# Kernel optimization log

Hardware: AMD Instinct MI355X
Metric: run time of the kernel (lower is better)

## Reference

```python
import jax, jax.numpy as jnp
import numpy as np

HEADS = 8
DIM_HEAD = 32
DIM = 256
HIDDEN = HEADS * DIM_HEAD  # 256


def setup_inputs() -> dict:
    key = jax.random.key(0)
    ks = jax.random.split(key, 6)
    B, T, C, H, W = 4, 16, DIM, 32, 32
    x = jax.random.normal(ks[0], (B, T, C, H, W), dtype=jnp.float32)
    rel_pos = jax.random.normal(ks[1], (HEADS, T, T), dtype=jnp.float32)
    # 1x1 conv weights == channel-mixing matrices
    w_qkv = jax.random.normal(ks[2], (3 * HIDDEN, C), dtype=jnp.float32) * (C ** -0.5)
    b_qkv = jnp.zeros((3 * HIDDEN,), dtype=jnp.float32)
    w_out = jax.random.normal(ks[3], (C, HIDDEN), dtype=jnp.float32) * (HIDDEN ** -0.5)
    b_out = jnp.zeros((C,), dtype=jnp.float32)
    return {"x": x, "rel_pos": rel_pos, "w_qkv": w_qkv, "b_qkv": b_qkv,
            "w_out": w_out, "b_out": b_out}


def reference(x, rel_pos, w_qkv, b_qkv, w_out, b_out):
    B, T, C, H, W = x.shape
    scale = DIM_HEAD ** -0.5
    # 1x1 conv QKV projection: (B,T,C,H,W) x (3*hidden, C) -> (B,T,H,W,3*hidden)
    qkv = jnp.einsum('btchw,oc->bthwo', x, w_qkv) + b_qkv
    q, k, v = jnp.split(qkv, 3, axis=-1)
    # split heads: (B,T,H,W,heads,dim_head); attention over T per (b,h,w,head)
    q = q.reshape(B, T, H, W, HEADS, DIM_HEAD) * scale
    k = k.reshape(B, T, H, W, HEADS, DIM_HEAD)
    v = v.reshape(B, T, H, W, HEADS, DIM_HEAD)
    # sim: (B,H,W,heads,T,T)
    sim = jnp.einsum('bihwnd,bjhwnd->bhwnij', q, k)
    sim = sim + rel_pos  # (heads,T,T) broadcasts over (B,H,W)
    attn = jax.nn.softmax(sim, axis=-1)
    out = jnp.einsum('bhwnij,bjhwnd->bihwnd', attn, v)  # (B,T,H,W,heads,dh)
    out = out.reshape(B, T, H, W, HIDDEN)
    # 1x1 conv output projection back to C channels
    y = jnp.einsum('bthwe,ce->bthwc', out, w_out) + b_out
    return jnp.transpose(y, (0, 1, 4, 2, 3))  # (B,T,C,H,W)
```

## Files before the change

kernel.cpp:

```cpp
#include <hip/hip_runtime.h>
#include <hip/hip_bf16.h>

typedef __attribute__((ext_vector_type(8))) short bf16x8;
typedef __attribute__((ext_vector_type(4))) float f32x4;
typedef __attribute__((ext_vector_type(16))) float f32x16;

namespace {

__device__ __forceinline__ unsigned short f2bf(float f) {
  unsigned int x;
  __builtin_memcpy(&x, &f, 4);
  x += 0x7fff + ((x >> 16) & 1);
  return (unsigned short)(x >> 16);
}
__device__ __forceinline__ unsigned int pack2(float a, float b) {
  return (unsigned int)f2bf(a) | ((unsigned int)f2bf(b) << 16);
}

constexpr int kWBStride = 264;
constexpr int kWBTile = 32 * kWBStride;
constexpr int kWB = 2 * kWBTile;
constexpr int kSite = 1920;
constexpr int kSmem = kWB + 8 * kSite;
constexpr int kPanelStride = 72;
constexpr int kWTileOff = 17408;
static_assert(kSmem * 2 <= 65536, "LDS budget");
static_assert(16 * 16 * kPanelStride <= kSmem, "x panel fits");
static_assert(512 * 17 * 4 <= kSmem * 2, "fbuf fits");
static_assert(kWTileOff + kWBTile <= kSmem, "wout tile fits after fbuf");

__global__ __launch_bounds__(512, 1) void attn_fused(
    const float* __restrict__ x,
    const float* __restrict__ rel,
    const float* __restrict__ wqkv,
    const float* __restrict__ bqkv,
    const float* __restrict__ wout,
    const float* __restrict__ bout,
    float* __restrict__ out) {
  __shared__ __align__(16) unsigned short smem[kSmem];
  const int tid = threadIdx.x;
  const int lane = tid & 63;
  const int wave = tid >> 6;
  const int quad = lane >> 4;
  const int lrow = lane & 15;
  const int half = lane >> 5;
  const int n32 = lane & 31;
  const int b = blockIdx.x >> 6;
  const int hw0 = (blockIdx.x & 63) * 16;

  const int wrow = tid >> 4;
  const int wcol = (tid & 15) * 16;
  float4 pw[4];
  {
    const float* sp = wqkv + (size_t)wrow * 256 + wcol;
#pragma unroll
    for (int u = 0; u < 4; ++u) pw[u] = *(const float4*)(sp + u * 4);
  }

  bf16x8 ax[16];
  {
    unsigned short* panel = smem;
    const int sloc = wave * 2 + (n32 >> 4);
#pragma unroll
    for (int cc4 = 0; cc4 < 4; ++cc4) {
      const int c0 = cc4 * 64;
      __syncthreads();
#pragma unroll
      for (int u = 0; u < 8; ++u) {
        const int idx = u * 512 + tid;
        const int row = idx >> 2;
        const int q = idx & 3;
        const int t = row >> 6;
        const int cl = row & 63;
        const float4 v = *(const float4*)(
            x + (((size_t)(b * 16 + t) * 256 + c0 + cl) << 10) + hw0 + q * 4);
        unsigned short* pr = panel + (t * 16 + q * 4) * kPanelStride + cl;
        pr[0] = f2bf(v.x);
        pr[kPanelStride] = f2bf(v.y);
        pr[2 * kPanelStride] = f2bf(v.z);
        pr[3 * kPanelStride] = f2bf(v.w);
      }
      __syncthreads();
#pragma unroll
      for (int kk = 0; kk < 4; ++kk)
        ax[cc4 * 4 + kk] = *(const bf16x8*)(
            panel + (lrow * 16 + sloc) * kPanelStride + kk * 16 + half * 8);
    }
  }

  unsigned short* qb = smem + kWB + wave * kSite;
  unsigned short* kb = qb + 640;
  unsigned short* vt = qb + 1280;

  const f32x4 zero4 = {0.f, 0.f, 0.f, 0.f};
  const float scale = 0.17677669529663687f;
  bf16x8 ao[2][8];

  auto qkv_tile = [&](int g, float bias) -> f32x16 {
    __syncthreads();
    unsigned short* WBc = smem + (g & 1) * kWBTile;
    {
      unsigned short* dst = WBc + wrow * kWBStride + wcol;
      uint4 a, bq;
      a.x = pack2(pw[0].x, pw[0].y);
      a.y = pack2(pw[0].z, pw[0].w);
      a.z = pack2(pw[1].x, pw[1].y);
      a.w = pack2(pw[1].z, pw[1].w);
      bq.x = pack2(pw[2].x, pw[2].y);
      bq.y = pack2(pw[2].z, pw[2].w);
      bq.z = pack2(pw[3].x, pw[3].y);
      bq.w = pack2(pw[3].z, pw[3].w);
      *(uint4*)dst = a;
      *(uint4*)(dst + 8) = bq;
    }
    {
      const int gn = g + 1;
      const int rowbase = (gn % 3) * 256 + (gn / 3) * 32;
      const float* sp = wqkv + (size_t)(rowbase + wrow) * 256 + wcol;
#pragma unroll
      for (int u = 0; u < 4; ++u) pw[u] = *(const float4*)(sp + u * 4);
    }
    __syncthreads();
    f32x16 accA, accB;
#pragma unroll
    for (int i = 0; i < 16; ++i) { accA[i] = bias; accB[i] = 0.f; }
    const unsigned short* br = WBc + n32 * kWBStride + half * 8;
#pragma unroll
    for (int kp = 0; kp < 8; ++kp) {
      const bf16x8 bfa = *(const bf16x8*)(br + (2 * kp) * 16);
      const bf16x8 bfb = *(const bf16x8*)(br + (2 * kp + 1) * 16);
      accA = __builtin_amdgcn_mfma_f32_32x32x16_bf16(ax[2 * kp], bfa, accA, 0, 0, 0);
      accB = __builtin_amdgcn_mfma_f32_32x32x16_bf16(ax[2 * kp + 1], bfb, accB, 0, 0, 0);
    }
#pragma unroll
    for (int i = 0; i < 16; ++i) accA[i] += accB[i];
    return accA;
  };

  auto head_body = [&](int h) {
    const f32x16 qacc = qkv_tile(h * 3 + 0, bqkv[h * 32 + n32]);
    const f32x16 kacc = qkv_tile(h * 3 + 1, bqkv[256 + h * 32 + n32]);
    const f32x16 vacc = qkv_tile(h * 3 + 2, bqkv[512 + h * 32 + n32]);
    float rl[4];
#pragma unroll
    for (int r = 0; r < 4; ++r) rl[r] = rel[h * 256 + (quad * 4 + r) * 16 + lrow];

#pragma unroll
    for (int s = 0; s < 2; ++s) {
#pragma unroll
      for (int rr = 0; rr < 8; ++rr) {
        const int t = (rr & 3) + 8 * (rr >> 2) + 4 * half;
        qb[t * 40 + n32] = f2bf(qacc[8 * s + rr]);
        kb[t * 40 + n32] = f2bf(kacc[8 * s + rr]);
      }
#pragma unroll
      for (int rp = 0; rp < 4; ++rp) {
        const int rr = rp * 2;
        const int t = (rr & 3) + 8 * (rr >> 2) + 4 * half;
        *(unsigned int*)&vt[n32 * 20 + t] =
            pack2(vacc[8 * s + rr], vacc[8 * s + rr + 1]);
      }
      const bf16x8 qf = *(const bf16x8*)(qb + lrow * 40 + quad * 8);
      const bf16x8 kf = *(const bf16x8*)(kb + lrow * 40 + quad * 8);
      const f32x4 sim = __builtin_amdgcn_mfma_f32_16x16x32_bf16(qf, kf, zero4, 0, 0, 0);
      float p[4], inv[4];
#pragma unroll
      for (int r = 0; r < 4; ++r) {
        const float v = sim[r] * scale + rl[r];
        float m = v;
        for (int off = 8; off; off >>= 1) m = fmaxf(m, __shfl_xor(m, off));
        const float e = __expf(v - m);
        float sum = e;
        for (int off = 8; off; off >>= 1) sum += __shfl_xor(sum, off);
        p[r] = e;
        inv[r] = 1.0f / sum;
      }
      unsigned short* pb = kb;
#pragma unroll
      for (int r = 0; r < 4; ++r) pb[(quad * 4 + r) * 24 + lrow] = f2bf(p[r]);
      bf16x8 pf, vf0, vf1;
      if (quad < 2) {
        pf = *(const bf16x8*)(pb + lrow * 24 + quad * 8);
        vf0 = *(const bf16x8*)(vt + lrow * 20 + quad * 8);
        vf1 = *(const bf16x8*)(vt + (16 + lrow) * 20 + quad * 8);
      } else {
#pragma unroll
        for (int j = 0; j < 8; ++j) { pf[j] = 0; vf0[j] = 0; vf1[j] = 0; }
      }
      const f32x4 o0 = __builtin_amdgcn_mfma_f32_16x16x32_bf16(pf, vf0, zero4, 0, 0, 0);
      const f32x4 o1 = __builtin_amdgcn_mfma_f32_16x16x32_bf16(pf, vf1, zero4, 0, 0, 0);
#pragma unroll
      for (int r = 0; r < 4; ++r) {
        const int t = quad * 4 + r;
        qb[t * 40 + lrow] = f2bf(o0[r] * inv[r]);
        qb[t * 40 + 16 + lrow] = f2bf(o1[r] * inv[r]);
      }
      ao[s][h] = *(const bf16x8*)(qb + lrow * 40 + quad * 8);
    }
  };

  head_body(0);
  head_body(1);
  head_body(2);
  head_body(3);
  head_body(4);
  head_body(5);
  head_body(6);
  head_body(7);

  __syncthreads();
  float* fbuf = (float*)smem;
  unsigned short* wtile = smem + kWTileOff;
  float* ob = out + ((size_t)b << 22);
#pragma unroll 1
  for (int cc = 0; cc < 8; ++cc) {
    {
      const float* sp = wout + (size_t)(cc * 32 + wrow) * 256 + wcol;
      const float4 v0 = ((const float4*)sp)[0];
      const float4 v1 = ((const float4*)sp)[1];
      const float4 v2 = ((const float4*)sp)[2];
      const float4 v3 = ((const float4*)sp)[3];
      uint4 a, bq;
      a.x = pack2(v0.x, v0.y);
      a.y = pack2(v0.z, v0.w);
      a.z = pack2(v1.x, v1.y);
      a.w = pack2(v1.z, v1.w);
      bq.x = pack2(v2.x, v2.y);
      bq.y = pack2(v2.z, v2.w);
      bq.z = pack2(v3.x, v3.y);
      bq.w = pack2(v3.z, v3.w);
      unsigned short* d = wtile + wrow * kWBStride + wcol;
      *(uint4*)d = a;
      *(uint4*)(d + 8) = bq;
    }
    __syncthreads();
#pragma unroll
    for (int sub = 0; sub < 2; ++sub) {
      const int c = cc * 32 + sub * 16 + lrow;
      const float bias = bout[c];
      f32x4 y0 = {bias, bias, bias, bias};
      f32x4 y1 = {bias, bias, bias, bias};
      const unsigned short* wrow_p = wtile + (sub * 16 + lrow) * kWBStride;
#pragma unroll
      for (int ks = 0; ks < 8; ++ks) {
        const bf16x8 wf = *(const bf16x8*)(wrow_p + ks * 32 + quad * 8);
        y0 = __builtin_amdgcn_mfma_f32_16x16x32_bf16(ao[0][ks], wf, y0, 0, 0, 0);
        y1 = __builtin_amdgcn_mfma_f32_16x16x32_bf16(ao[1][ks], wf, y1, 0, 0, 0);
      }
#pragma unroll
      for (int r = 0; r < 4; ++r) {
        const int t = quad * 4 + r;
        const int L = (t * 32 + sub * 16 + lrow) * 17 + wave * 2;
        fbuf[L] = y0[r];
        fbuf[L + 1] = y1[r];
      }
    }
    __syncthreads();
    {
      const int t = tid >> 5, cl = tid & 31;
      float v[16];
#pragma unroll
      for (int i = 0; i < 16; ++i) v[i] = fbuf[tid * 17 + i];
      float* dst = ob + ((size_t)(t * 256 + cc * 32 + cl)) * 1024 + hw0;
#pragma unroll
      for (int u = 0; u < 4; ++u) {
        float4 q;
        q.x = v[u * 4]; q.y = v[u * 4 + 1]; q.z = v[u * 4 + 2]; q.w = v[u * 4 + 3];
        *(float4*)(dst + u * 4) = q;
      }
    }
    __syncthreads();
  }
}

}

extern "C" void kernel_launch(void* const* d_in, const int* in_sizes, int n_in,
                              void* d_out, int out_size, void* d_ws, size_t ws_size,
                              hipStream_t stream) {
  const float* x = (const float*)d_in[0];
  const float* rel = (const float*)d_in[1];
  const float* wqkv = (const float*)d_in[2];
  const float* bqkv = (const float*)d_in[3];
  const float* wout = (const float*)d_in[4];
  const float* bout = (const float*)d_in[5];
  float* out = (float*)d_out;
  (void)in_sizes; (void)n_in; (void)out_size; (void)d_ws; (void)ws_size;

  attn_fused<<<256, 512, 0, stream>>>(x, rel, wqkv, bqkv, wout, bout, out);
}
```

Measured before the change: 202.5 us.

## Pre-convert weights to bf16 workspace and read MFMA operands directly from L2

After: 261.2 us. 29.0% more time.

```diff
diff --git a/kernel.cpp b/kernel.cpp
--- a/kernel.cpp
+++ b/kernel.cpp
@@ -17,25 +17,236 @@
   return (unsigned int)f2bf(a) | ((unsigned int)f2bf(b) << 16);
 }
 
+__global__ __launch_bounds__(256) void wprep(const float* __restrict__ wqkv,
+                                             const float* __restrict__ wout,
+                                             unsigned short* __restrict__ wAll) {
+  const int g = blockIdx.x;
+  const int tid = threadIdx.x;
+  const int row_l = tid >> 3;
+  const int seg = tid & 7;
+  const float* src;
+  int srow;
+  if (g < 24) { src = wqkv; srow = (g % 3) * 256 + (g / 3) * 32 + row_l; }
+  else        { src = wout; srow = (g - 24) * 32 + row_l; }
+  const float* s = src + (size_t)srow * 256 + seg * 32;
+  unsigned short* d = wAll + ((size_t)(g * 32 + row_l)) * 256 + seg * 32;
+#pragma unroll
+  for (int u = 0; u < 8; ++u) {
+    const float4 v = *(const float4*)(s + u * 4);
+    uint2 p;
+    p.x = pack2(v.x, v.y);
+    p.y = pack2(v.z, v.w);
+    *(uint2*)(d + u * 4) = p;
+  }
+}
+
+constexpr int kPanelStride = 72;
+constexpr int kPanel = 16 * 16 * kPanelStride;
+constexpr int kSiteL = 1920;
+constexpr int kSmemL = kPanel + 8 * kSiteL;
+static_assert(512 * 17 * 4 <= kPanel * 2, "fbuf fits in panel region");
+
+__global__ __launch_bounds__(512, 1) void attn_l2w(
+    const float* __restrict__ x,
+    const float* __restrict__ rel,
+    const unsigned short* __restrict__ wAll,
+    const float* __restrict__ bqkv,
+    const float* __restrict__ bout,
+    float* __restrict__ out) {
+  __shared__ __align__(16) unsigned short smem[kSmemL];
+  const int tid = threadIdx.x;
+  const int lane = tid & 63;
+  const int wave = tid >> 6;
+  const int quad = lane >> 4;
+  const int lrow = lane & 15;
+  const int half = lane >> 5;
+  const int n32 = lane & 31;
+  const int b = blockIdx.x >> 6;
+  const int hw0 = (blockIdx.x & 63) * 16;
+
+  bf16x8 ax[16];
+  {
+    unsigned short* panel = smem;
+    const int sloc = wave * 2 + (n32 >> 4);
+#pragma unroll
+    for (int cc4 = 0; cc4 < 4; ++cc4) {
+      const int c0 = cc4 * 64;
+      __syncthreads();
+#pragma unroll
+      for (int u = 0; u < 8; ++u) {
+        const int idx = u * 512 + tid;
+        const int row = idx >> 2;
+        const int q = idx & 3;
+        const int t = row >> 6;
+        const int cl = row & 63;
+        const float4 v = *(const float4*)(
+            x + (((size_t)(b * 16 + t) * 256 + c0 + cl) << 10) + hw0 + q * 4);
+        unsigned short* pr = panel + (t * 16 + q * 4) * kPanelStride + cl;
+        pr[0] = f2bf(v.x);
+        pr[kPanelStride] = f2bf(v.y);
+        pr[2 * kPanelStride] = f2bf(v.z);
+        pr[3 * kPanelStride] = f2bf(v.w);
+      }
+      __syncthreads();
+#pragma unroll
+      for (int kk = 0; kk < 4; ++kk)
+        ax[cc4 * 4 + kk] = *(const bf16x8*)(
+            panel + (lrow * 16 + sloc) * kPanelStride + kk * 16 + half * 8);
+    }
+  }
+
+  unsigned short* qb = smem + kPanel + wave * kSiteL;
+  unsigned short* kb = qb + 640;
+  unsigned short* vt = qb + 1280;
+
+  const f32x4 zero4 = {0.f, 0.f, 0.f, 0.f};
+  const float scale = 0.17677669529663687f;
+  bf16x8 ao[2][8];
+
+  auto qkv_tile = [&](int g, float bias) -> f32x16 {
+    f32x16 accA, accB;
+#pragma unroll
+    for (int i = 0; i < 16; ++i) { accA[i] = bias; accB[i] = 0.f; }
+    const unsigned short* br = wAll + (((size_t)(g * 32 + n32)) << 8) + half * 8;
+#pragma unroll
+    for (int kp = 0; kp < 8; ++kp) {
+      const bf16x8 bfa = *(const bf16x8*)(br + (2 * kp) * 16);
+      const bf16x8 bfb = *(const bf16x8*)(br + (2 * kp + 1) * 16);
+      accA = __builtin_amdgcn_mfma_f32_32x32x16_bf16(ax[2 * kp], bfa, accA, 0, 0, 0);
+      accB = __builtin_amdgcn_mfma_f32_32x32x16_bf16(ax[2 * kp + 1], bfb, accB, 0, 0, 0);
+    }
+#pragma unroll
+    for (int i = 0; i < 16; ++i) accA[i] += accB[i];
+    return accA;
+  };
+
+  auto head_body = [&](int h) {
+    const f32x16 qacc = qkv_tile(h * 3 + 0, bqkv[h * 32 + n32]);
+    const f32x16 kacc = qkv_tile(h * 3 + 1, bqkv[256 + h * 32 + n32]);
+    const f32x16 vacc = qkv_tile(h * 3 + 2, bqkv[512 + h * 32 + n32]);
+    float rl[4];
+#pragma unroll
+    for (int r = 0; r < 4; ++r) rl[r] = rel[h * 256 + (quad * 4 + r) * 16 + lrow];
+
+#pragma unroll
+    for (int s = 0; s < 2; ++s) {
+#pragma unroll
+      for (int rr = 0; rr < 8; ++rr) {
+        const int t = (rr & 3) + 8 * (rr >> 2) + 4 * half;
+        qb[t * 40 + n32] = f2bf(qacc[8 * s + rr]);
+        kb[t * 40 + n32] = f2bf(kacc[8 * s + rr]);
+      }
+#pragma unroll
+      for (int rp = 0; rp < 4; ++rp) {
+        const int rr = rp * 2;
+        const int t = (rr & 3) + 8 * (rr >> 2) + 4 * half;
+        *(unsigned int*)&vt[n32 * 20 + t] =
+            pack2(vacc[8 * s + rr], vacc[8 * s + rr + 1]);
+      }
+      const bf16x8 qf = *(const bf16x8*)(qb + lrow * 40 + quad * 8);
+      const bf16x8 kf = *(const bf16x8*)(kb + lrow * 40 + quad * 8);
+      const f32x4 sim = __builtin_amdgcn_mfma_f32_16x16x32_bf16(qf, kf, zero4, 0, 0, 0);
+      float p[4], inv[4];
+#pragma unroll
+      for (int r = 0; r < 4; ++r) {
+        const float v = sim[r] * scale + rl[r];
+        float m = v;
+        for (int off = 8; off; off >>= 1) m = fmaxf(m, __shfl_xor(m, off));
+        const float e = __expf(v - m);
+        float sum = e;
+        for (int off = 8; off; off >>= 1) sum += __shfl_xor(sum, off);
+        p[r] = e;
+        inv[r] = 1.0f / sum;
+      }
+      unsigned short* pb = kb;
+#pragma unroll
+      for (int r = 0; r < 4; ++r) pb[(quad * 4 + r) * 24 + lrow] = f2bf(p[r]);
+      bf16x8 pf, vf0, vf1;
+      if (quad < 2) {
+        pf = *(const bf16x8*)(pb + lrow * 24 + quad * 8);
+        vf0 = *(const bf16x8*)(vt + lrow * 20 + quad * 8);
+        vf1 = *(const bf16x8*)(vt + (16 + lrow) * 20 + quad * 8);
+      } else {
+#pragma unroll
+        for (int j = 0; j < 8; ++j) { pf[j] = 0; vf0[j] = 0; vf1[j] = 0; }
+      }
+      const f32x4 o0 = __builtin_amdgcn_mfma_f32_16x16x32_bf16(pf, vf0, zero4, 0, 0, 0);
+      const f32x4 o1 = __builtin_amdgcn_mfma_f32_16x16x32_bf16(pf, vf1, zero4, 0, 0, 0);
+#pragma unroll
+      for (int r = 0; r < 4; ++r) {
+        const int t = quad * 4 + r;
+        qb[t * 40 + lrow] = f2bf(o0[r] * inv[r]);
+        qb[t * 40 + 16 + lrow] = f2bf(o1[r] * inv[r]);
+      }
+      ao[s][h] = *(const bf16x8*)(qb + lrow * 40 + quad * 8);
+    }
+  };
+
+  head_body(0);
+  head_body(1);
+  head_body(2);
+  head_body(3);
+  head_body(4);
+  head_body(5);
+  head_body(6);
+  head_body(7);
+
+  __syncthreads();
+  float* fbuf = (float*)smem;
+  float* ob = out + ((size_t)b << 22);
+#pragma unroll 1
+  for (int cc = 0; cc < 8; ++cc) {
+#pragma unroll
+    for (int sub = 0; sub < 2; ++sub) {
+      const int c = cc * 32 + sub * 16 + lrow;
+      const float bias = bout[c];
+      f32x4 y0 = {bias, bias, bias, bias};
+      f32x4 y1 = {bias, bias, bias, bias};
+#pragma unroll
+      for (int ks = 0; ks < 8; ++ks) {
+        const bf16x8 wf =
+            *(const bf16x8*)(wAll + (size_t)(768 + c) * 256 + ks * 32 + quad * 8);
+        y0 = __builtin_amdgcn_mfma_f32_16x16x32_bf16(ao[0][ks], wf, y0, 0, 0, 0);
+        y1 = __builtin_amdgcn_mfma_f32_16x16x32_bf16(ao[1][ks], wf, y1, 0, 0, 0);
+      }
+#pragma unroll
+      for (int r = 0; r < 4; ++r) {
+        const int t = quad * 4 + r;
+        const int L = (t * 32 + sub * 16 + lrow) * 17 + wave * 2;
+        fbuf[L] = y0[r];
+        fbuf[L + 1] = y1[r];
+      }
+    }
+    __syncthreads();
+    {
+      const int t = tid >> 5, cl = tid & 31;
+      float v[16];
+#pragma unroll
+      for (int i = 0; i < 16; ++i) v[i] = fbuf[tid * 17 + i];
+      float* dst = ob + ((size_t)(t * 256 + cc * 32 + cl)) * 1024 + hw0;
+#pragma unroll
+      for (int u = 0; u < 4; ++u) {
+        float4 q;
+        q.x = v[u * 4]; q.y = v[u * 4 + 1]; q.z = v[u * 4 + 2]; q.w = v[u * 4 + 3];
+        *(float4*)(dst + u * 4) = q;
+      }
+    }
+    __syncthreads();
+  }
+}
+
 constexpr int kWBStride = 264;
 constexpr int kWBTile = 32 * kWBStride;
 constexpr int kWB = 2 * kWBTile;
 constexpr int kSite = 1920;
 constexpr int kSmem = kWB + 8 * kSite;
-constexpr int kPanelStride = 72;
 constexpr int kWTileOff = 17408;
-static_assert(kSmem * 2 <= 65536, "LDS budget");
-static_assert(16 * 16 * kPanelStride <= kSmem, "x panel fits");
-static_assert(512 * 17 * 4 <= kSmem * 2, "fbuf fits");
-static_assert(kWTileOff + kWBTile <= kSmem, "wout tile fits after fbuf");
+static_assert(kSmem * 2 <= 160 * 1024, "LDS budget");
 
 __global__ __launch_bounds__(512, 1) void attn_fused(
-    const float* __restrict__ x,
-    const float* __restrict__ rel,
-    const float* __restrict__ wqkv,
-    const float* __restrict__ bqkv,
-    const float* __restrict__ wout,
-    const float* __restrict__ bout,
+    const float* __restrict__ x, const float* __restrict__ rel,
+    const float* __restrict__ wqkv, const float* __restrict__ bqkv,
+    const float* __restrict__ wout, const float* __restrict__ bout,
     float* __restrict__ out) {
   __shared__ __align__(16) unsigned short smem[kSmem];
   const int tid = threadIdx.x;
@@ -285,7 +496,14 @@
   const float* wout = (const float*)d_in[4];
   const float* bout = (const float*)d_in[5];
   float* out = (float*)d_out;
-  (void)in_sizes; (void)n_in; (void)out_size; (void)d_ws; (void)ws_size;
-
-  attn_fused<<<256, 512, 0, stream>>>(x, rel, wqkv, bqkv, wout, bout, out);
-}
+  (void)in_sizes; (void)n_in; (void)out_size;
+
+  constexpr size_t kWAllBytes = (size_t)1024 * 256 * sizeof(unsigned short);
+  if (ws_size >= kWAllBytes) {
+    unsigned short* wAll = (unsigned short*)d_ws;
+    wprep<<<32, 256, 0, stream>>>(wqkv, wout, wAll);
+    attn_l2w<<<256, 512, 0, stream>>>(x, rel, wAll, bqkv, bout, out);
+  } else {
+    attn_fused<<<256, 512, 0, stream>>>(x, rel, wqkv, bqkv, wout, bout, out);
+  }
+}
```

## Use 1024-thread blocks with one spatial site per wave and 16x16 MFMAs

Applied to the files above, without the earlier changes.

Result: no change. 203.3 us (+0.4%).

```diff
diff --git a/kernel.cpp b/kernel.cpp
--- a/kernel.cpp
+++ b/kernel.cpp
@@ -3,7 +3,6 @@
 
 typedef __attribute__((ext_vector_type(8))) short bf16x8;
 typedef __attribute__((ext_vector_type(4))) float f32x4;
-typedef __attribute__((ext_vector_type(16))) float f32x16;
 
 namespace {
 
@@ -20,16 +19,16 @@
 constexpr int kWBStride = 264;
 constexpr int kWBTile = 32 * kWBStride;
 constexpr int kWB = 2 * kWBTile;
-constexpr int kSite = 1920;
-constexpr int kSmem = kWB + 8 * kSite;
+constexpr int kSite = 1792;
+constexpr int kSmem = kWB + 16 * kSite;
 constexpr int kPanelStride = 72;
-constexpr int kWTileOff = 17408;
-static_assert(kSmem * 2 <= 65536, "LDS budget");
+constexpr int kWTileOff = 34816;
+static_assert(kSmem * 2 <= 160 * 1024, "LDS budget");
 static_assert(16 * 16 * kPanelStride <= kSmem, "x panel fits");
 static_assert(512 * 17 * 4 <= kSmem * 2, "fbuf fits");
 static_assert(kWTileOff + kWBTile <= kSmem, "wout tile fits after fbuf");
 
-__global__ __launch_bounds__(512, 1) void attn_fused(
+__global__ __launch_bounds__(1024, 4) void attn_fused(
     const float* __restrict__ x,
     const float* __restrict__ rel,
     const float* __restrict__ wqkv,
@@ -43,31 +42,28 @@
   const int wave = tid >> 6;
   const int quad = lane >> 4;
   const int lrow = lane & 15;
-  const int half = lane >> 5;
-  const int n32 = lane & 31;
   const int b = blockIdx.x >> 6;
   const int hw0 = (blockIdx.x & 63) * 16;
 
-  const int wrow = tid >> 4;
-  const int wcol = (tid & 15) * 16;
-  float4 pw[4];
+  const int wrow = tid >> 5;
+  const int wcol = (tid & 31) * 8;
+  float4 pw[2];
   {
     const float* sp = wqkv + (size_t)wrow * 256 + wcol;
-#pragma unroll
-    for (int u = 0; u < 4; ++u) pw[u] = *(const float4*)(sp + u * 4);
+    pw[0] = ((const float4*)sp)[0];
+    pw[1] = ((const float4*)sp)[1];
   }
 
-  bf16x8 ax[16];
+  bf16x8 ax[8];
   {
     unsigned short* panel = smem;
-    const int sloc = wave * 2 + (n32 >> 4);
 #pragma unroll
     for (int cc4 = 0; cc4 < 4; ++cc4) {
       const int c0 = cc4 * 64;
       __syncthreads();
 #pragma unroll
-      for (int u = 0; u < 8; ++u) {
-        const int idx = u * 512 + tid;
+      for (int u = 0; u < 4; ++u) {
+        const int idx = u * 1024 + tid;
         const int row = idx >> 2;
         const int q = idx & 3;
         const int t = row >> 6;
@@ -82,121 +78,112 @@
       }
       __syncthreads();
 #pragma unroll
-      for (int kk = 0; kk < 4; ++kk)
-        ax[cc4 * 4 + kk] = *(const bf16x8*)(
-            panel + (lrow * 16 + sloc) * kPanelStride + kk * 16 + half * 8);
+      for (int kk = 0; kk < 2; ++kk)
+        ax[cc4 * 2 + kk] = *(const bf16x8*)(
+            panel + (lrow * 16 + wave) * kPanelStride + kk * 32 + quad * 8);
     }
   }
 
   unsigned short* qb = smem + kWB + wave * kSite;
-  unsigned short* kb = qb + 640;
-  unsigned short* vt = qb + 1280;
+  unsigned short* kbuf = qb + 512;
+  unsigned short* vtb = qb + 1024;
+  unsigned short* pb = qb + 1536;
 
   const f32x4 zero4 = {0.f, 0.f, 0.f, 0.f};
   const float scale = 0.17677669529663687f;
-  bf16x8 ao[2][8];
-
-  auto qkv_tile = [&](int g, float bias) -> f32x16 {
+  bf16x8 ao[8];
+
+  auto qkv_tile = [&](int g, int h, int sel) {
     __syncthreads();
     unsigned short* WBc = smem + (g & 1) * kWBTile;
     {
-      unsigned short* dst = WBc + wrow * kWBStride + wcol;
-      uint4 a, bq;
+      uint4 a;
       a.x = pack2(pw[0].x, pw[0].y);
       a.y = pack2(pw[0].z, pw[0].w);
       a.z = pack2(pw[1].x, pw[1].y);
       a.w = pack2(pw[1].z, pw[1].w);
-      bq.x = pack2(pw[2].x, pw[2].y);
-      bq.y = pack2(pw[2].z, pw[2].w);
-      bq.z = pack2(pw[3].x, pw[3].y);
-      bq.w = pack2(pw[3].z, pw[3].w);
-      *(uint4*)dst = a;
-      *(uint4*)(dst + 8) = bq;
+      *(uint4*)(WBc + wrow * kWBStride + wcol) = a;
     }
     {
       const int gn = g + 1;
       const int rowbase = (gn % 3) * 256 + (gn / 3) * 32;
       const float* sp = wqkv + (size_t)(rowbase + wrow) * 256 + wcol;
-#pragma unroll
-      for (int u = 0; u < 4; ++u) pw[u] = *(const float4*)(sp + u * 4);
-    }
-    __syncthreads();
-    f32x16 accA, accB;
-#pragma unroll
-    for (int i = 0; i < 16; ++i) { accA[i] = bias; accB[i] = 0.f; }
-    const unsigned short* br = WBc + n32 * kWBStride + half * 8;
-#pragma unroll
-    for (int kp = 0; kp < 8; ++kp) {
-      const bf16x8 bfa = *(const bf16x8*)(br + (2 * kp) * 16);
-      const bf16x8 bfb = *(const bf16x8*)(br + (2 * kp + 1) * 16);
-      accA = __builtin_amdgcn_mfma_f32_32x32x16_bf16(ax[2 * kp], bfa, accA, 0, 0, 0);
-      accB = __builtin_amdgcn_mfma_f32_32x32x16_bf16(ax[2 * kp + 1], bfb, accB, 0, 0, 0);
-    }
-#pragma unroll
-    for (int i = 0; i < 16; ++i) accA[i] += accB[i];
-    return accA;
+      pw[0] = ((const float4*)sp)[0];
+      pw[1] = ((const float4*)sp)[1];
+    }
+    __syncthreads();
+    const float bias0 = bqkv[sel * 256 + h * 32 + lrow];
+    const float bias1 = bqkv[sel * 256 + h * 32 + 16 + lrow];
+    f32x4 acc0 = {bias0, bias0, bias0, bias0};
+    f32x4 acc1 = {bias1, bias1, bias1, bias1};
+#pragma unroll
+    for (int ks = 0; ks < 8; ++ks) {
+      const bf16x8 b0 =
+          *(const bf16x8*)(WBc + lrow * kWBStride + ks * 32 + quad * 8);
+      const bf16x8 b1 =
+          *(const bf16x8*)(WBc + (16 + lrow) * kWBStride + ks * 32 + quad * 8);
+      acc0 = __builtin_amdgcn_mfma_f32_16x16x32_bf16(ax[ks], b0, acc0, 0, 0, 0);
+      acc1 = __builtin_amdgcn_mfma_f32_16x16x32_bf16(ax[ks], b1, acc1, 0, 0, 0);
+    }
+    if (sel < 2) {
+      unsigned short* dst = sel ? kbuf : qb;
+#pragma unroll
+      for (int r = 0; r < 4; ++r) {
+        const int row = quad * 4 + r;
+        dst[row * 32 + lrow] = f2bf(acc0[r]);
+        dst[row * 32 + 16 + lrow] = f2bf(acc1[r]);
+      }
+    } else {
+#pragma unroll
+      for (int r = 0; r < 4; ++r) {
+        const int row = quad * 4 + r;
+        vtb[lrow * 16 + row] = f2bf(acc0[r]);
+        vtb[(16 + lrow) * 16 + row] = f2bf(acc1[r]);
+      }
+    }
   };
 
   auto head_body = [&](int h) {
-    const f32x16 qacc = qkv_tile(h * 3 + 0, bqkv[h * 32 + n32]);
-    const f32x16 kacc = qkv_tile(h * 3 + 1, bqkv[256 + h * 32 + n32]);
-    const f32x16 vacc = qkv_tile(h * 3 + 2, bqkv[512 + h * 32 + n32]);
-    float rl[4];
-#pragma unroll
-    for (int r = 0; r < 4; ++r) rl[r] = rel[h * 256 + (quad * 4 + r) * 16 + lrow];
-
-#pragma unroll
-    for (int s = 0; s < 2; ++s) {
-#pragma unroll
-      for (int rr = 0; rr < 8; ++rr) {
-        const int t = (rr & 3) + 8 * (rr >> 2) + 4 * half;
-        qb[t * 40 + n32] = f2bf(qacc[8 * s + rr]);
-        kb[t * 40 + n32] = f2bf(kacc[8 * s + rr]);
-      }
-#pragma unroll
-      for (int rp = 0; rp < 4; ++rp) {
-        const int rr = rp * 2;
-        const int t = (rr & 3) + 8 * (rr >> 2) + 4 * half;
-        *(unsigned int*)&vt[n32 * 20 + t] =
-            pack2(vacc[8 * s + rr], vacc[8 * s + rr + 1]);
-      }
-      const bf16x8 qf = *(const bf16x8*)(qb + lrow * 40 + quad * 8);
-      const bf16x8 kf = *(const bf16x8*)(kb + lrow * 40 + quad * 8);
-      const f32x4 sim = __builtin_amdgcn_mfma_f32_16x16x32_bf16(qf, kf, zero4, 0, 0, 0);
-      float p[4], inv[4];
-#pragma unroll
-      for (int r = 0; r < 4; ++r) {
-        const float v = sim[r] * scale + rl[r];
-        float m = v;
-        for (int off = 8; off; off >>= 1) m = fmaxf(m, __shfl_xor(m, off));
-        const float e = __expf(v - m);
-        float sum = e;
-        for (int off = 8; off; off >>= 1) sum += __shfl_xor(sum, off);
-        p[r] = e;
-        inv[r] = 1.0f / sum;
-      }
-      unsigned short* pb = kb;
-#pragma unroll
-      for (int r = 0; r < 4; ++r) pb[(quad * 4 + r) * 24 + lrow] = f2bf(p[r]);
-      bf16x8 pf, vf0, vf1;
-      if (quad < 2) {
-        pf = *(const bf16x8*)(pb + lrow * 24 + quad * 8);
-        vf0 = *(const bf16x8*)(vt + lrow * 20 + quad * 8);
-        vf1 = *(const bf16x8*)(vt + (16 + lrow) * 20 + quad * 8);
-      } else {
-#pragma unroll
-        for (int j = 0; j < 8; ++j) { pf[j] = 0; vf0[j] = 0; vf1[j] = 0; }
-      }
-      const f32x4 o0 = __builtin_amdgcn_mfma_f32_16x16x32_bf16(pf, vf0, zero4, 0, 0, 0);
-      const f32x4 o1 = __builtin_amdgcn_mfma_f32_16x16x32_bf16(pf, vf1, zero4, 0, 0, 0);
-#pragma unroll
-      for (int r = 0; r < 4; ++r) {
-        const int t = quad * 4 + r;
-        qb[t * 40 + lrow] = f2bf(o0[r] * inv[r]);
-        qb[t * 40 + 16 + lrow] = f2bf(o1[r] * inv[r]);
-      }
-      ao[s][h] = *(const bf16x8*)(qb + lrow * 40 + quad * 8);
-    }
+    qkv_tile(h * 3 + 0, h, 0);
+    qkv_tile(h * 3 + 1, h, 1);
+    qkv_tile(h * 3 + 2, h, 2);
+
+    const bf16x8 qf = *(const bf16x8*)&qb[lrow * 32 + quad * 8];
+    const bf16x8 kf = *(const bf16x8*)&kbuf[lrow * 32 + quad * 8];
+    const f32x4 sim = __builtin_amdgcn_mfma_f32_16x16x32_bf16(qf, kf, zero4, 0, 0, 0);
+    float p[4], inv[4];
+#pragma unroll
+    for (int r = 0; r < 4; ++r) {
+      const int i = quad * 4 + r;
+      const float v = sim[r] * scale + rel[h * 256 + i * 16 + lrow];
+      float m = v;
+      for (int off = 8; off; off >>= 1) m = fmaxf(m, __shfl_xor(m, off));
+      const float e = __expf(v - m);
+      float s = e;
+      for (int off = 8; off; off >>= 1) s += __shfl_xor(s, off);
+      p[r] = e;
+      inv[r] = 1.0f / s;
+    }
+#pragma unroll
+    for (int r = 0; r < 4; ++r) pb[(quad * 4 + r) * 16 + lrow] = f2bf(p[r]);
+    bf16x8 pf, vf0, vf1;
+    if (quad < 2) {
+      pf = *(const bf16x8*)&pb[lrow * 16 + quad * 8];
+      vf0 = *(const bf16x8*)&vtb[lrow * 16 + quad * 8];
+      vf1 = *(const bf16x8*)&vtb[(16 + lrow) * 16 + quad * 8];
+    } else {
+#pragma unroll
+      for (int j = 0; j < 8; ++j) { pf[j] = 0; vf0[j] = 0; vf1[j] = 0; }
+    }
+    const f32x4 o0 = __builtin_amdgcn_mfma_f32_16x16x32_bf16(pf, vf0, zero4, 0, 0, 0);
+    const f32x4 o1 = __builtin_amdgcn_mfma_f32_16x16x32_bf16(pf, vf1, zero4, 0, 0, 0);
+#pragma unroll
+    for (int r = 0; r < 4; ++r) {
+      const int t = quad * 4 + r;
+      qb[t * 32 + lrow] = f2bf(o0[r] * inv[r]);
+      qb[t * 32 + 16 + lrow] = f2bf(o1[r] * inv[r]);
+    }
+    ao[h] = *(const bf16x8*)&qb[lrow * 32 + quad * 8];
   };
 
   head_body(0);
@@ -218,56 +205,44 @@
       const float* sp = wout + (size_t)(cc * 32 + wrow) * 256 + wcol;
       const float4 v0 = ((const float4*)sp)[0];
       const float4 v1 = ((const float4*)sp)[1];
-      const float4 v2 = ((const float4*)sp)[2];
-      const float4 v3 = ((const float4*)sp)[3];
-      uint4 a, bq;
+      uint4 a;
       a.x = pack2(v0.x, v0.y);
       a.y = pack2(v0.z, v0.w);
       a.z = pack2(v1.x, v1.y);
       a.w = pack2(v1.z, v1.w);
-      bq.x = pack2(v2.x, v2.y);
-      bq.y = pack2(v2.z, v2.w);
-      bq.z = pack2(v3.x, v3.y);
-      bq.w = pack2(v3.z, v3.w);
-      unsigned short* d = wtile + wrow * kWBStride + wcol;
-      *(uint4*)d = a;
-      *(uint4*)(d + 8) = bq;
+      *(uint4*)(wtile + wrow * kWBStride + wcol) = a;
     }
     __syncthreads();
 #pragma unroll
     for (int sub = 0; sub < 2; ++sub) {
       const int c = cc * 32 + sub * 16 + lrow;
       const float bias = bout[c];
-      f32x4 y0 = {bias, bias, bias, bias};
-      f32x4 y1 = {bias, bias, bias, bias};
-      const unsigned short* wrow_p = wtile + (sub * 16 + lrow) * kWBStride;
+      f32x4 y = {bias, bias, bias, bias};
+      const unsigned short* wrp = wtile + (sub * 16 + lrow) * kWBStride;
 #pragma unroll
       for (int ks = 0; ks < 8; ++ks) {
-        const bf16x8 wf = *(const bf16x8*)(wrow_p + ks * 32 + quad * 8);
-        y0 = __builtin_amdgcn_mfma_f32_16x16x32_bf16(ao[0][ks], wf, y0, 0, 0, 0);
-        y1 = __builtin_amdgcn_mfma_f32_16x16x32_bf16(ao[1][ks], wf, y1, 0, 0, 0);
+        const bf16x8 wf = *(const bf16x8*)(wrp + ks * 32 + quad * 8);
+        y = __builtin_amdgcn_mfma_f32_16x16x32_bf16(ao[ks], wf, y, 0, 0, 0);
       }
 #pragma unroll
       for (int r = 0; r < 4; ++r) {
         const int t = quad * 4 + r;
-        const int L = (t * 32 + sub * 16 + lrow) * 17 + wave * 2;
-        fbuf[L] = y0[r];
-        fbuf[L + 1] = y1[r];
-      }
-    }
-    __syncthreads();
-    {
-      const int t = tid >> 5, cl = tid & 31;
-      float v[16];
-#pragma unroll
-      for (int i = 0; i < 16; ++i) v[i] = fbuf[tid * 17 + i];
-      float* dst = ob + ((size_t)(t * 256 + cc * 32 + cl)) * 1024 + hw0;
-#pragma unroll
-      for (int u = 0; u < 4; ++u) {
-        float4 q;
-        q.x = v[u * 4]; q.y = v[u * 4 + 1]; q.z = v[u * 4 + 2]; q.w = v[u * 4 + 3];
-        *(float4*)(dst + u * 4) = q;
-      }
+        fbuf[(t * 32 + sub * 16 + lrow) * 17 + wave] = y[r];
+      }
+    }
+    __syncthreads();
+    {
+      const int L = tid >> 1, hf = tid & 1;
+      const int t = L >> 5, cl = L & 31;
+      float v[8];
+#pragma unroll
+      for (int i = 0; i < 8; ++i) v[i] = fbuf[L * 17 + hf * 8 + i];
+      float* dst = ob + ((size_t)(t * 256 + cc * 32 + cl)) * 1024 + hw0 + hf * 8;
+      float4 s0, s1;
+      s0.x = v[0]; s0.y = v[1]; s0.z = v[2]; s0.w = v[3];
+      s1.x = v[4]; s1.y = v[5]; s1.z = v[6]; s1.w = v[7];
+      *(float4*)dst = s0;
+      *(float4*)(dst + 4) = s1;
     }
     __syncthreads();
   }
@@ -287,5 +262,5 @@
   float* out = (float*)d_out;
   (void)in_sizes; (void)n_in; (void)out_size; (void)d_ws; (void)ws_size;
 
-  attn_fused<<<256, 512, 0, stream>>>(x, rel, wqkv, bqkv, wout, bout, out);
-}
+  attn_fused<<<256, 1024, 0, stream>>>(x, rel, wqkv, bqkv, wout, bout, out);
+}
```
